# Kernel tuning notes

Measured on AMD Instinct MI355X. Metric: run time of the kernel, lower is better.

The kernel has to match this reference:

```python
import jax, jax.numpy as jnp
import numpy as np

N_NODES = 100000
N_EDGES = 3200000
N_GRAPHS = 1024


def _glorot(key, shape):
    fan_in, fan_out = shape[0], shape[1]
    lim = jnp.sqrt(6.0 / (fan_in + fan_out))
    return jax.random.uniform(key, shape, minval=-lim, maxval=lim, dtype=jnp.float32)


def setup_inputs() -> dict:
    key = jax.random.key(0)
    ks = jax.random.split(key, 9)
    x = jax.random.normal(ks[0], (N_NODES, 3), dtype=jnp.float32)
    edge_index = jax.random.randint(ks[1], (2, N_EDGES), 0, N_NODES, dtype=jnp.int64)
    batch = jnp.sort(jax.random.randint(ks[2], (N_NODES,), 0, N_GRAPHS, dtype=jnp.int64))
    return {
        "x": x,
        "edge_index": edge_index,
        "batch": batch,
        "W1": _glorot(ks[3], (3, 16)),
        "b1": jnp.zeros((16,), jnp.float32),
        "W2": _glorot(ks[4], (16, 16)),
        "b2": jnp.zeros((16,), jnp.float32),
        "Wl": _glorot(ks[5], (16, 7)),
        "bl": jnp.zeros((7,), jnp.float32),
    }


def gcn_conv(x, edge_index, W, b, num_nodes):
    """GCNConv with normalize=True, add_self_loops=True (PyG defaults)."""
    x = x @ W  # linear transform first: [N, F_out]
    loop = jnp.arange(num_nodes, dtype=edge_index.dtype)
    row = jnp.concatenate([edge_index[0], loop])  # source nodes
    col = jnp.concatenate([edge_index[1], loop])  # target nodes
    # degree of target nodes (edge weight 1 incl. self loops)
    deg = jax.ops.segment_sum(jnp.ones_like(col, dtype=x.dtype), col,
                              num_segments=num_nodes)
    dinv = jnp.where(deg > 0, jax.lax.rsqrt(deg), 0.0)
    norm = dinv[row] * dinv[col]  # [E+N]
    msg = x[row] * norm[:, None]  # gather + normalize
    out = jax.ops.segment_sum(msg, col, num_segments=num_nodes)  # scatter-add
    return out + b


def reference(x, edge_index, batch, W1, b1, W2, b2, Wl, bl):
    h = jax.nn.relu(gcn_conv(x, edge_index, W1, b1, N_NODES))
    h = gcn_conv(h, edge_index, W2, b2, N_NODES)
    pooled = jax.ops.segment_sum(h, batch, num_segments=N_GRAPHS)  # global_add_pool
    logits = pooled @ Wl + bl  # [G, 7]
    return jax.nn.log_softmax(logits, axis=1)
```

## Files before the change

kernel.cpp:

```cpp
#include <hip/hip_runtime.h>
#include <hip/hip_fp16.h>
#include <math.h>

#define N_NODES  100000
#define N_EDGES  3200000
#define N_GRAPHS 1024
#define NBUCK    391
#define CAP      8960
#define NPS      1024
#define ECH      3125

__device__ inline unsigned pack2(float a, float b) {
    union { __half2 h; unsigned u; } c;
    c.h = __floats2half2_rn(a, b);
    return c.u;
}
__device__ inline float2 up2(unsigned u) {
    union { unsigned u; __half2 h; } c; c.u = u;
    return __half22float2(c.h);
}
__device__ inline void acc8(float* a, uint4 v) {
    float2 f;
    f = up2(v.x); a[0] += f.x; a[1] += f.y;
    f = up2(v.y); a[2] += f.x; a[3] += f.y;
    f = up2(v.z); a[4] += f.x; a[5] += f.y;
    f = up2(v.w); a[6] += f.x; a[7] += f.y;
}
__device__ inline void acc4(float* a, uint2 v) {
    float2 f;
    f = up2(v.x); a[0] += f.x; a[1] += f.y;
    f = up2(v.y); a[2] += f.x; a[3] += f.y;
}

__global__ void k_pair_scatter(const int* __restrict__ row, const int* __restrict__ col,
                               int* __restrict__ gcursor, int* __restrict__ pairbuf) {
    __shared__ int            sbuf[ECH];
    __shared__ unsigned short sbk[ECH];
    __shared__ int            lhist[NBUCK];
    __shared__ int            lcur[NBUCK];
    __shared__ int            wbase[NBUCK];
    int t = threadIdx.x;
    int e0 = blockIdx.x * ECH;
    for (int j = t; j < NBUCK; j += 256) lhist[j] = 0;
    __syncthreads();
    for (int k = t; k < ECH; k += 256)
        atomicAdd(&lhist[col[e0 + k] >> 8], 1);
    __syncthreads();
    if (t < 64) {
        int carry = 0;
        for (int c0 = 0; c0 < NBUCK; c0 += 64) {
            int idx = c0 + t;
            int v = (idx < NBUCK) ? lhist[idx] : 0;
            int orig = v;
#pragma unroll
            for (int o = 1; o < 64; o <<= 1) {
                int u = __shfl_up(v, o, 64);
                if (t >= o) v += u;
            }
            if (idx < NBUCK) lcur[idx] = v - orig + carry;
            carry += __shfl(v, 63, 64);
        }
    }
    __syncthreads();
    for (int j = t; j < NBUCK; j += 256) {
        int c = lhist[j];
        int g = c ? atomicAdd(&gcursor[j], c) : 0;
        wbase[j] = j * CAP + g - lcur[j];
    }
    __syncthreads();
    for (int k = t; k < ECH; k += 256) {
        int e = e0 + k;
        int c = col[e];
        int bk = c >> 8;
        int pos = atomicAdd(&lcur[bk], 1);
        sbuf[pos] = row[e] | ((c & 255) << 17);
        sbk[pos] = (unsigned short)bk;
    }
    __syncthreads();
    for (int k = t; k < ECH; k += 256) {
        int bk = sbk[k];
        int pos = wbase[bk] + k;
        if (pos < (bk + 1) * CAP)
            pairbuf[pos] = sbuf[k];
    }
}

__global__ void k_finalize(int* __restrict__ pairbuf, const int* __restrict__ gcursor,
                           int2* __restrict__ rowse, float* __restrict__ dinv,
                           const float* __restrict__ x, const float* __restrict__ W1,
                           __half* __restrict__ bufA16) {
    __shared__ int slice[CAP];
    __shared__ int lcnt[256];
    __shared__ int ls[256];
    __shared__ int cur[256];
    __shared__ float sw1[48];
    int t = threadIdx.x, b = blockIdx.x;
    int base = b * CAP;
    int cnt_b = gcursor[b];
    if (cnt_b > CAP) cnt_b = CAP;
    lcnt[t] = 0;
    if (t < 48) sw1[t] = W1[t];
    for (int k = t; k < cnt_b; k += 256) slice[k] = pairbuf[base + k];
    __syncthreads();
    for (int k = t; k < cnt_b; k += 256)
        atomicAdd(&lcnt[(slice[k] >> 17) & 255], 1);
    __syncthreads();
    int myc = lcnt[t];
    ls[t] = myc;
    __syncthreads();
    for (int o = 1; o < 256; o <<= 1) {
        int v = (t >= o) ? ls[t - o] : 0;
        __syncthreads();
        ls[t] += v;
        __syncthreads();
    }
    int node = (b << 8) + t;
    int st = base + ls[t] - myc;
    cur[t] = st;
    if (node < N_NODES) {
        rowse[node] = make_int2(st, st + myc);
        float d = rsqrtf((float)(myc + 1));
        dinv[node] = d;
        float x0 = x[node * 3 + 0], x1 = x[node * 3 + 1], x2 = x[node * 3 + 2];
        float v[16];
#pragma unroll
        for (int j = 0; j < 16; j++)
            v[j] = (x0 * sw1[j] + x1 * sw1[16 + j] + x2 * sw1[32 + j]) * d;
        uint4 u0 = { pack2(v[0], v[1]), pack2(v[2], v[3]), pack2(v[4], v[5]), pack2(v[6], v[7]) };
        uint4 u1 = { pack2(v[8], v[9]), pack2(v[10], v[11]), pack2(v[12], v[13]), pack2(v[14], v[15]) };
        uint4* p = (uint4*)(bufA16 + (long long)node * 16);
        p[0] = u0; p[1] = u1;
    }
    __syncthreads();
    for (int k = t; k < cnt_b; k += 256) {
        int p = slice[k];
        int pos = atomicAdd(&cur[(p >> 17) & 255], 1);
        pairbuf[pos] = p & 0x1FFFF;
    }
}

__global__ void k_gather1(const uint4* __restrict__ src16, const int* __restrict__ csr,
                          const int2* __restrict__ rowse, const float* __restrict__ dinv,
                          const float* __restrict__ b1, const float* __restrict__ W2,
                          __half* __restrict__ out16) {
    __shared__ float sh[128][17];
    __shared__ float sW[256];
    __shared__ float sb1[16];
    int t = threadIdx.x;
    sW[t] = W2[t];
    if (t < 16) sb1[t] = b1[t];
    int local = t >> 1, h = t & 1;
    int node = blockIdx.x * 128 + local;
    bool act = node < N_NODES;
    int2 se = act ? rowse[node] : make_int2(0, 0);
    int s = se.x, e = se.y;
    float acc[8] = {0, 0, 0, 0, 0, 0, 0, 0};
    if (act) {
        uint4 u = src16[node * 2 + h];
        float2 f;
        f = up2(u.x); acc[0] = f.x; acc[1] = f.y;
        f = up2(u.y); acc[2] = f.x; acc[3] = f.y;
        f = up2(u.z); acc[4] = f.x; acc[5] = f.y;
        f = up2(u.w); acc[6] = f.x; acc[7] = f.y;
    }
    int j = s;
    for (; j + 8 <= e; j += 8) {
        int i0 = csr[j],     i1 = csr[j + 1], i2 = csr[j + 2], i3 = csr[j + 3];
        int i4 = csr[j + 4], i5 = csr[j + 5], i6 = csr[j + 6], i7 = csr[j + 7];
        uint4 v0 = src16[i0 * 2 + h], v1 = src16[i1 * 2 + h];
        uint4 v2 = src16[i2 * 2 + h], v3 = src16[i3 * 2 + h];
        uint4 v4 = src16[i4 * 2 + h], v5 = src16[i5 * 2 + h];
        uint4 v6 = src16[i6 * 2 + h], v7 = src16[i7 * 2 + h];
        acc8(acc, v0); acc8(acc, v1); acc8(acc, v2); acc8(acc, v3);
        acc8(acc, v4); acc8(acc, v5); acc8(acc, v6); acc8(acc, v7);
    }
    for (; j < e; j++) acc8(acc, src16[csr[j] * 2 + h]);
    float d = act ? dinv[node] : 0.f;
#pragma unroll
    for (int k = 0; k < 8; k++) {
        float v = acc[k] * d + sb1[h * 8 + k];
        sh[local][h * 8 + k] = v > 0.f ? v : 0.f;
    }
    __syncthreads();
    float v[8];
#pragma unroll
    for (int jj = 0; jj < 8; jj++) {
        int jo = h * 8 + jj;
        float a = 0.f;
#pragma unroll
        for (int k = 0; k < 16; k++) a += sh[local][k] * sW[k * 16 + jo];
        v[jj] = a * d;
    }
    if (act) {
        uint4 u = { pack2(v[0], v[1]), pack2(v[2], v[3]), pack2(v[4], v[5]), pack2(v[6], v[7]) };
        ((uint4*)(out16 + (long long)node * 16 + h * 8))[0] = u;
    }
}

__global__ void k_gather2(const uint2* __restrict__ src16, const int* __restrict__ csr,
                          const int2* __restrict__ rowse, const float* __restrict__ dinv,
                          float* __restrict__ dst) {
    int t = threadIdx.x;
    int node = blockIdx.x * 64 + (t >> 2);
    int h = t & 3;
    if (node >= N_NODES) return;
    int2 se = rowse[node];
    int s = se.x, e = se.y;
    float acc[4];
    {
        uint2 u = src16[node * 4 + h];
        float2 f;
        f = up2(u.x); acc[0] = f.x; acc[1] = f.y;
        f = up2(u.y); acc[2] = f.x; acc[3] = f.y;
    }
    int j = s;
    for (; j + 8 <= e; j += 8) {
        int i0 = csr[j],     i1 = csr[j + 1], i2 = csr[j + 2], i3 = csr[j + 3];
        int i4 = csr[j + 4], i5 = csr[j + 5], i6 = csr[j + 6], i7 = csr[j + 7];
        uint2 v0 = src16[i0 * 4 + h], v1 = src16[i1 * 4 + h];
        uint2 v2 = src16[i2 * 4 + h], v3 = src16[i3 * 4 + h];
        uint2 v4 = src16[i4 * 4 + h], v5 = src16[i5 * 4 + h];
        uint2 v6 = src16[i6 * 4 + h], v7 = src16[i7 * 4 + h];
        acc4(acc, v0); acc4(acc, v1); acc4(acc, v2); acc4(acc, v3);
        acc4(acc, v4); acc4(acc, v5); acc4(acc, v6); acc4(acc, v7);
    }
    for (; j < e; j++) acc4(acc, src16[csr[j] * 4 + h]);
    float d = dinv[node];
    float4 o = { acc[0] * d, acc[1] * d, acc[2] * d, acc[3] * d };
    ((float4*)(dst + (long long)node * 16 + h * 4))[0] = o;
}

__global__ void k_pool_head(const float* __restrict__ agg2, const int* __restrict__ batch,
                            const float* __restrict__ b2, const float* __restrict__ Wl,
                            const float* __restrict__ bl, float* __restrict__ out) {
    int g = blockIdx.x;
    int t = threadIdx.x;
    __shared__ int range[2];
    __shared__ float part[64];
    __shared__ float pooled[16];
    __shared__ float logits[7];
    if (t < 2) {
        int target = g + t;
        int lo = 0, hi = N_NODES;
        while (lo < hi) {
            int mid = (lo + hi) >> 1;
            if (batch[mid] < target) lo = mid + 1; else hi = mid;
        }
        range[t] = lo;
    }
    __syncthreads();
    int s = range[0], e = range[1];
    int f = t & 15, chunk = t >> 4;
    float acc = 0.f;
    for (int i = s + chunk; i < e; i += 4) acc += agg2[(long long)i * 16 + f];
    part[t] = acc;
    __syncthreads();
    if (t < 16) {
        float p = part[t] + part[t + 16] + part[t + 32] + part[t + 48];
        pooled[t] = p + (float)(e - s) * b2[t];
    }
    __syncthreads();
    if (t < 7) {
        float a = bl[t];
#pragma unroll
        for (int k = 0; k < 16; k++) a += pooled[k] * Wl[k * 7 + t];
        logits[t] = a;
    }
    __syncthreads();
    if (t == 0) {
        float m = logits[0];
#pragma unroll
        for (int c = 1; c < 7; c++) m = fmaxf(m, logits[c]);
        float sum = 0.f;
#pragma unroll
        for (int c = 0; c < 7; c++) sum += expf(logits[c] - m);
        float lse = logf(sum) + m;
#pragma unroll
        for (int c = 0; c < 7; c++) out[g * 7 + c] = logits[c] - lse;
    }
}

extern "C" void kernel_launch(void* const* d_in, const int* in_sizes, int n_in,
                              void* d_out, int out_size, void* d_ws, size_t ws_size,
                              hipStream_t stream) {
    const float* x     = (const float*)d_in[0];
    const int*   ei    = (const int*)d_in[1];
    const int*   batch = (const int*)d_in[2];
    const float* W1    = (const float*)d_in[3];
    const float* b1    = (const float*)d_in[4];
    const float* W2    = (const float*)d_in[5];
    const float* b2    = (const float*)d_in[6];
    const float* Wl    = (const float*)d_in[7];
    const float* bl    = (const float*)d_in[8];
    float* out = (float*)d_out;

    const int* row = ei;
    const int* col = ei + N_EDGES;

    int*    gcursor = (int*)d_ws;
    float*  dinv    = (float*)d_ws + 400;
    int2*   rowse   = (int2*)((int*)d_ws + 100400);
    int*    pairbuf = (int*)d_ws + 300400;
    __half* bufA16  = (__half*)((int*)d_ws + 3803760);
    __half* bufB16  = (__half*)((int*)d_ws + 4603760);
    float*  bufB    = (float*)d_ws + 5403760;

    const int BT = 256;

    hipMemsetAsync(gcursor, 0, 400 * sizeof(int), stream);
    k_pair_scatter<<<NPS, BT, 0, stream>>>(row, col, gcursor, pairbuf);
    k_finalize<<<NBUCK, BT, 0, stream>>>(pairbuf, gcursor, rowse, dinv, x, W1, bufA16);
    k_gather1<<<(N_NODES + 127) / 128, BT, 0, stream>>>((const uint4*)bufA16, pairbuf, rowse,
                                                        dinv, b1, W2, bufB16);
    k_gather2<<<(N_NODES + 63) / 64, BT, 0, stream>>>((const uint2*)bufB16, pairbuf, rowse,
                                                      dinv, bufB);
    k_pool_head<<<N_GRAPHS, 64, 0, stream>>>(bufB, batch, b2, Wl, bl, out);
}
```

Before: 230.3 us.

## Fuse graph pooling into second gather, halve bucket width and gather1 blocks

Global add pooling moves into the second aggregation kernel. Each block accumulates per-graph partial sums in shared memory and flushes them with global atomics, so the float node buffer is no longer written and re-read by a separate pool kernel. The bucket sort now uses 128-node buckets (twice as many, smaller capacity, fewer scatter blocks with larger edge chunks), and the first gather runs 128-thread blocks over 64 nodes. This removes a full intermediate pass but adds float atomics whose summation order is nondeterministic, and it relies on the sorted batch assumption.

```diff
diff --git a/kernel.cpp b/kernel.cpp
--- a/kernel.cpp
+++ b/kernel.cpp
@@ -5,10 +5,10 @@
 #define N_NODES  100000
 #define N_EDGES  3200000
 #define N_GRAPHS 1024
-#define NBUCK    391
-#define CAP      8960
-#define NPS      1024
-#define ECH      3125
+#define NBUCK    782
+#define CAP      4608
+#define NPS      512
+#define ECH      6250
 
 __device__ inline unsigned pack2(float a, float b) {
     union { __half2 h; unsigned u; } c;
@@ -44,7 +44,7 @@
     for (int j = t; j < NBUCK; j += 256) lhist[j] = 0;
     __syncthreads();
     for (int k = t; k < ECH; k += 256)
-        atomicAdd(&lhist[col[e0 + k] >> 8], 1);
+        atomicAdd(&lhist[col[e0 + k] >> 7], 1);
     __syncthreads();
     if (t < 64) {
         int carry = 0;
@@ -71,9 +71,9 @@
     for (int k = t; k < ECH; k += 256) {
         int e = e0 + k;
         int c = col[e];
-        int bk = c >> 8;
+        int bk = c >> 7;
         int pos = atomicAdd(&lcur[bk], 1);
-        sbuf[pos] = row[e] | ((c & 255) << 17);
+        sbuf[pos] = row[e] | ((c & 127) << 17);
         sbk[pos] = (unsigned short)bk;
     }
     __syncthreads();
@@ -90,51 +90,53 @@
                            const float* __restrict__ x, const float* __restrict__ W1,
                            __half* __restrict__ bufA16) {
     __shared__ int slice[CAP];
-    __shared__ int lcnt[256];
-    __shared__ int ls[256];
-    __shared__ int cur[256];
+    __shared__ int lcnt[128];
+    __shared__ int ls[128];
+    __shared__ int cur[128];
     __shared__ float sw1[48];
     int t = threadIdx.x, b = blockIdx.x;
     int base = b * CAP;
     int cnt_b = gcursor[b];
     if (cnt_b > CAP) cnt_b = CAP;
-    lcnt[t] = 0;
+    if (t < 128) lcnt[t] = 0;
     if (t < 48) sw1[t] = W1[t];
     for (int k = t; k < cnt_b; k += 256) slice[k] = pairbuf[base + k];
     __syncthreads();
     for (int k = t; k < cnt_b; k += 256)
-        atomicAdd(&lcnt[(slice[k] >> 17) & 255], 1);
-    __syncthreads();
-    int myc = lcnt[t];
-    ls[t] = myc;
-    __syncthreads();
-    for (int o = 1; o < 256; o <<= 1) {
-        int v = (t >= o) ? ls[t - o] : 0;
+        atomicAdd(&lcnt[(slice[k] >> 17) & 127], 1);
+    __syncthreads();
+    int myc = (t < 128) ? lcnt[t] : 0;
+    if (t < 128) ls[t] = myc;
+    __syncthreads();
+    for (int o = 1; o < 128; o <<= 1) {
+        int v = (t < 128 && t >= o) ? ls[t - o] : 0;
         __syncthreads();
-        ls[t] += v;
+        if (t < 128) ls[t] += v;
         __syncthreads();
     }
-    int node = (b << 8) + t;
-    int st = base + ls[t] - myc;
-    cur[t] = st;
-    if (node < N_NODES) {
-        rowse[node] = make_int2(st, st + myc);
-        float d = rsqrtf((float)(myc + 1));
-        dinv[node] = d;
-        float x0 = x[node * 3 + 0], x1 = x[node * 3 + 1], x2 = x[node * 3 + 2];
-        float v[16];
-#pragma unroll
-        for (int j = 0; j < 16; j++)
-            v[j] = (x0 * sw1[j] + x1 * sw1[16 + j] + x2 * sw1[32 + j]) * d;
-        uint4 u0 = { pack2(v[0], v[1]), pack2(v[2], v[3]), pack2(v[4], v[5]), pack2(v[6], v[7]) };
-        uint4 u1 = { pack2(v[8], v[9]), pack2(v[10], v[11]), pack2(v[12], v[13]), pack2(v[14], v[15]) };
-        uint4* p = (uint4*)(bufA16 + (long long)node * 16);
-        p[0] = u0; p[1] = u1;
+    int node = (b << 7) + t;
+    if (t < 128) {
+        int st = base + ls[t] - myc;
+        cur[t] = st;
+        if (node < N_NODES) {
+            rowse[node] = make_int2(st, st + myc);
+            float d = rsqrtf((float)(myc + 1));
+            dinv[node] = d;
+            float x0 = x[node * 3 + 0], x1 = x[node * 3 + 1], x2 = x[node * 3 + 2];
+            float v[16];
+#pragma unroll
+            for (int j = 0; j < 16; j++)
+                v[j] = (x0 * sw1[j] + x1 * sw1[16 + j] + x2 * sw1[32 + j]) * d;
+            uint4 u0 = { pack2(v[0], v[1]), pack2(v[2], v[3]), pack2(v[4], v[5]), pack2(v[6], v[7]) };
+            uint4 u1 = { pack2(v[8], v[9]), pack2(v[10], v[11]), pack2(v[12], v[13]), pack2(v[14], v[15]) };
+            uint4* p = (uint4*)(bufA16 + (long long)node * 16);
+            p[0] = u0; p[1] = u1;
+        }
     }
     __syncthreads();
     for (int k = t; k < cnt_b; k += 256) {
         int p = slice[k];
-        int pos = atomicAdd(&cur[(p >> 17) & 255], 1);
+        int pos = atomicAdd(&cur[(p >> 17) & 127], 1);
         pairbuf[pos] = p & 0x1FFFF;
     }
 }
@@ -143,14 +145,14 @@
                           const int2* __restrict__ rowse, const float* __restrict__ dinv,
                           const float* __restrict__ b1, const float* __restrict__ W2,
                           __half* __restrict__ out16) {
-    __shared__ float sh[128][17];
+    __shared__ float sh[64][17];
     __shared__ float sW[256];
     __shared__ float sb1[16];
     int t = threadIdx.x;
-    sW[t] = W2[t];
+    sW[t] = W2[t]; sW[t + 128] = W2[t + 128];
     if (t < 16) sb1[t] = b1[t];
     int local = t >> 1, h = t & 1;
-    int node = blockIdx.x * 128 + local;
+    int node = blockIdx.x * 64 + local;
     bool act = node < N_NODES;
     int2 se = act ? rowse[node] : make_int2(0, 0);
     int s = se.x, e = se.y;
@@ -199,45 +201,69 @@
 
 __global__ void k_gather2(const uint2* __restrict__ src16, const int* __restrict__ csr,
                           const int2* __restrict__ rowse, const float* __restrict__ dinv,
-                          float* __restrict__ dst) {
+                          const int* __restrict__ batch, float* __restrict__ pooled) {
+    __shared__ float pl[8][16];
+    __shared__ int ginfo[2];
     int t = threadIdx.x;
-    int node = blockIdx.x * 64 + (t >> 2);
+    int node0 = blockIdx.x * 64;
+    if (t < 128) pl[t >> 4][t & 15] = 0.f;
+    if (t == 0) {
+        int last = node0 + 63; if (last >= N_NODES) last = N_NODES - 1;
+        ginfo[0] = batch[node0];
+        ginfo[1] = batch[last];
+    }
+    __syncthreads();
+    int node = node0 + (t >> 2);
     int h = t & 3;
-    if (node >= N_NODES) return;
-    int2 se = rowse[node];
-    int s = se.x, e = se.y;
-    float acc[4];
-    {
+    float o[4] = {0, 0, 0, 0};
+    bool act = node < N_NODES;
+    int slot = 0;
+    if (act) {
+        int2 se = rowse[node];
+        int s = se.x, e = se.y;
         uint2 u = src16[node * 4 + h];
         float2 f;
-        f = up2(u.x); acc[0] = f.x; acc[1] = f.y;
-        f = up2(u.y); acc[2] = f.x; acc[3] = f.y;
-    }
-    int j = s;
-    for (; j + 8 <= e; j += 8) {
-        int i0 = csr[j],     i1 = csr[j + 1], i2 = csr[j + 2], i3 = csr[j + 3];
-        int i4 = csr[j + 4], i5 = csr[j + 5], i6 = csr[j + 6], i7 = csr[j + 7];
-        uint2 v0 = src16[i0 * 4 + h], v1 = src16[i1 * 4 + h];
-        uint2 v2 = src16[i2 * 4 + h], v3 = src16[i3 * 4 + h];
-        uint2 v4 = src16[i4 * 4 + h], v5 = src16[i5 * 4 + h];
-        uint2 v6 = src16[i6 * 4 + h], v7 = src16[i7 * 4 + h];
-        acc4(acc, v0); acc4(acc, v1); acc4(acc, v2); acc4(acc, v3);
-        acc4(acc, v4); acc4(acc, v5); acc4(acc, v6); acc4(acc, v7);
-    }
-    for (; j < e; j++) acc4(acc, src16[csr[j] * 4 + h]);
-    float d = dinv[node];
-    float4 o = { acc[0] * d, acc[1] * d, acc[2] * d, acc[3] * d };
-    ((float4*)(dst + (long long)node * 16 + h * 4))[0] = o;
-}
-
-__global__ void k_pool_head(const float* __restrict__ agg2, const int* __restrict__ batch,
-                            const float* __restrict__ b2, const float* __restrict__ Wl,
-                            const float* __restrict__ bl, float* __restrict__ out) {
+        f = up2(u.x); o[0] = f.x; o[1] = f.y;
+        f = up2(u.y); o[2] = f.x; o[3] = f.y;
+        int j = s;
+        for (; j + 8 <= e; j += 8) {
+            int i0 = csr[j],     i1 = csr[j + 1], i2 = csr[j + 2], i3 = csr[j + 3];
+            int i4 = csr[j + 4], i5 = csr[j + 5], i6 = csr[j + 6], i7 = csr[j + 7];
+            uint2 v0 = src16[i0 * 4 + h], v1 = src16[i1 * 4 + h];
+            uint2 v2 = src16[i2 * 4 + h], v3 = src16[i3 * 4 + h];
+            uint2 v4 = src16[i4 * 4 + h], v5 = src16[i5 * 4 + h];
+            uint2 v6 = src16[i6 * 4 + h], v7 = src16[i7 * 4 + h];
+            acc4(o, v0); acc4(o, v1); acc4(o, v2); acc4(o, v3);
+            acc4(o, v4); acc4(o, v5); acc4(o, v6); acc4(o, v7);
+        }
+        for (; j < e; j++) acc4(o, src16[csr[j] * 4 + h]);
+        float d = dinv[node];
+        o[0] *= d; o[1] *= d; o[2] *= d; o[3] *= d;
+        slot = batch[node] - ginfo[0];
+        if (slot < 8) {
+#pragma unroll
+            for (int k = 0; k < 4; k++) atomicAdd(&pl[slot][h * 4 + k], o[k]);
+        } else {
+#pragma unroll
+            for (int k = 0; k < 4; k++) atomicAdd(&pooled[batch[node] * 16 + h * 4 + k], o[k]);
+        }
+    }
+    __syncthreads();
+    if (t < 128) {
+        int s = t >> 4, f = t & 15;
+        int span = ginfo[1] - ginfo[0];
+        if (s <= span && s < 8)
+            atomicAdd(&pooled[(ginfo[0] + s) * 16 + f], pl[s][f]);
+    }
+}
+
+__global__ void k_head(const float* __restrict__ pooled, const int* __restrict__ batch,
+                       const float* __restrict__ b2, const float* __restrict__ Wl,
+                       const float* __restrict__ bl, float* __restrict__ out) {
     int g = blockIdx.x;
     int t = threadIdx.x;
     __shared__ int range[2];
-    __shared__ float part[64];
-    __shared__ float pooled[16];
+    __shared__ float pld[16];
     __shared__ float logits[7];
     if (t < 2) {
         int target = g + t;
@@ -249,21 +275,13 @@
         range[t] = lo;
     }
     __syncthreads();
-    int s = range[0], e = range[1];
-    int f = t & 15, chunk = t >> 4;
-    float acc = 0.f;
-    for (int i = s + chunk; i < e; i += 4) acc += agg2[(long long)i * 16 + f];
-    part[t] = acc;
-    __syncthreads();
-    if (t < 16) {
-        float p = part[t] + part[t + 16] + part[t + 32] + part[t + 48];
-        pooled[t] = p + (float)(e - s) * b2[t];
-    }
+    float cnt = (float)(range[1] - range[0]);
+    if (t < 16) pld[t] = pooled[g * 16 + t] + cnt * b2[t];
     __syncthreads();
     if (t < 7) {
         float a = bl[t];
 #pragma unroll
-        for (int k = 0; k < 16; k++) a += pooled[k] * Wl[k * 7 + t];
+        for (int k = 0; k < 16; k++) a += pld[k] * Wl[k * 7 + t];
         logits[t] = a;
     }
     __syncthreads();
@@ -298,21 +316,21 @@
     const int* col = ei + N_EDGES;
 
     int*    gcursor = (int*)d_ws;
-    float*  dinv    = (float*)d_ws + 400;
-    int2*   rowse   = (int2*)((int*)d_ws + 100400);
-    int*    pairbuf = (int*)d_ws + 300400;
-    __half* bufA16  = (__half*)((int*)d_ws + 3803760);
-    __half* bufB16  = (__half*)((int*)d_ws + 4603760);
-    float*  bufB    = (float*)d_ws + 5403760;
+    float*  pooled  = (float*)d_ws + 800;
+    float*  dinv    = (float*)d_ws + 17200;
+    int2*   rowse   = (int2*)((int*)d_ws + 117200);
+    int*    pairbuf = (int*)d_ws + 317200;
+    __half* bufA16  = (__half*)((int*)d_ws + 3920656);
+    __half* bufB16  = (__half*)((int*)d_ws + 4720656);
 
     const int BT = 256;
 
-    hipMemsetAsync(gcursor, 0, 400 * sizeof(int), stream);
+    hipMemsetAsync(gcursor, 0, 17184 * sizeof(int), stream);
     k_pair_scatter<<<NPS, BT, 0, stream>>>(row, col, gcursor, pairbuf);
     k_finalize<<<NBUCK, BT, 0, stream>>>(pairbuf, gcursor, rowse, dinv, x, W1, bufA16);
-    k_gather1<<<(N_NODES + 127) / 128, BT, 0, stream>>>((const uint4*)bufA16, pairbuf, rowse,
-                                                        dinv, b1, W2, bufB16);
+    k_gather1<<<(N_NODES + 63) / 64, 128, 0, stream>>>((const uint4*)bufA16, pairbuf, rowse,
+                                                       dinv, b1, W2, bufB16);
     k_gather2<<<(N_NODES + 63) / 64, BT, 0, stream>>>((const uint2*)bufB16, pairbuf, rowse,
-                                                      dinv, bufB);
-    k_pool_head<<<N_GRAPHS, 64, 0, stream>>>(bufB, batch, b2, Wl, bl, out);
-}
+                                                      dinv, batch, pooled);
+    k_head<<<N_GRAPHS, 64, 0, stream>>>(pooled, batch, b2, Wl, bl, out);
+}
```

Measured after the change: 213.9 us. -7.1%, faster.
